# Optimization experiments

Measured on AMD Instinct MI355X. Metric: run time of the kernel, lower is better.

The kernel has to match this reference:

```python
import jax, jax.numpy as jnp
import numpy as np

N_NODES = 100000
FT_IN = 128
NHID = 64
N_EDGES = 1000000


def setup_inputs() -> dict:
    key = jax.random.key(0)
    ks = jax.random.split(key, 9)
    seq = jax.random.normal(ks[0], (N_NODES, FT_IN), dtype=jnp.float32)
    row = jax.random.randint(ks[1], (N_EDGES,), 0, N_NODES, dtype=jnp.int32)
    col = jax.random.randint(ks[2], (N_EDGES,), 0, N_NODES, dtype=jnp.int32)
    # encoder: LogReg Linear(ft_in, nhid), xavier-uniform weight, zero bias
    lim_enc = float(np.sqrt(6.0 / (FT_IN + NHID)))
    W_enc = jax.random.uniform(ks[3], (NHID, FT_IN), jnp.float32, -lim_enc, lim_enc)
    b_enc = jnp.zeros((NHID,), jnp.float32)
    # decoder lin1: Linear(2*nhid, nhid)
    lim1 = float(1.0 / np.sqrt(2 * NHID))
    W1 = jax.random.uniform(ks[4], (NHID, 2 * NHID), jnp.float32, -lim1, lim1)
    b1 = jax.random.uniform(ks[5], (NHID,), jnp.float32, -lim1, lim1)
    # decoder lin2: Linear(nhid, 1)
    lim2 = float(1.0 / np.sqrt(NHID))
    W2 = jax.random.uniform(ks[6], (1, NHID), jnp.float32, -lim2, lim2)
    b2 = jax.random.uniform(ks[7], (1,), jnp.float32, -lim2, lim2)
    return {"seq": seq, "W_enc": W_enc, "b_enc": b_enc, "W1": W1, "b1": b1,
            "W2": W2, "b2": b2, "row": row, "col": col}


def reference(seq, W_enc, b_enc, W1, b1, W2, b2, row, col):
    # encoder: z_all = seq @ W_enc^T + b_enc   -> [N, nhid]
    z = seq @ W_enc.T + b_enc
    # edge gather + concat -> [E, 2*nhid]
    e = jnp.concatenate([z[row], z[col]], axis=-1)
    h = jax.nn.relu(e @ W1.T + b1)             # [E, nhid]
    out = h @ W2.T + b2                        # [E, 1]
    return out.reshape(-1)
```

## Files before the change

### kernel.cpp

```cpp
#include <hip/hip_runtime.h>
#include <hip/hip_bf16.h>


#define K_IN  128
#define N_OUT 128
#define LDB   136

typedef short bf16x8 __attribute__((ext_vector_type(8)));
typedef float f32x4  __attribute__((ext_vector_type(4)));
typedef _Float16 half8 __attribute__((ext_vector_type(8)));

static __device__ __forceinline__ short f2bf(float x) {
    __hip_bfloat16 h = __float2bfloat16(x);
    return *reinterpret_cast<short*>(&h);
}

__global__ __launch_bounds__(256) void prep_kernel(
        const float* __restrict__ W_enc, const float* __restrict__ b_enc,
        const float* __restrict__ W1,    const float* __restrict__ b1,
        __hip_bfloat16* __restrict__ Wb, float* __restrict__ bcat)
{
    int idx = blockIdx.x * blockDim.x + threadIdx.x;
    if (idx >= N_OUT * K_IN) return;
    int i = idx >> 7;
    int k = idx & 127;
    int irow = i & 63;
    int joff = (i < 64) ? 0 : 64;
    float s = 0.f;
    #pragma unroll 8
    for (int j = 0; j < 64; ++j)
        s = fmaf(W1[irow * 128 + joff + j], W_enc[j * 128 + k], s);
    Wb[i * K_IN + k] = __float2bfloat16(s);
    if (k == 0) {
        float b = 0.f;
        for (int j = 0; j < 64; ++j)
            b = fmaf(W1[irow * 128 + joff + j], b_enc[j], b);
        if (i < 64) b += b1[i];
        bcat[i] = b;
    }
}

__global__ __launch_bounds__(256) void node_proj_kernel(
        const float* __restrict__ seq, const __hip_bfloat16* __restrict__ Wb,
        const float* __restrict__ bcat, _Float16* __restrict__ UVh, int nNodes)
{
    __shared__ short Bs[N_OUT * LDB];

    int tid  = threadIdx.x;
    int base = blockIdx.x * 64;

    #pragma unroll
    for (int it = 0; it < 8; ++it) {
        int c8 = tid + 256 * it;
        int r  = c8 >> 4;
        int cb = (c8 & 15) * 8;
        *(int4*)(Bs + r * LDB + cb) = *(const int4*)(Wb + r * K_IN + cb);
    }
    __syncthreads();

    int lane = tid & 63;
    int w    = tid >> 6;
    int lr   = lane & 15;
    int lg   = lane >> 4;

    int arow = base + 16 * w + lr;
    if (arow >= nNodes) arow = nNodes - 1;
    const float* aptr = seq + (size_t)arow * K_IN + lg * 8;

    f32x4 acc[8];
    #pragma unroll
    for (int nt = 0; nt < 8; ++nt) {
        float b = bcat[nt * 16 + lr];
        acc[nt] = (f32x4){b, b, b, b};
    }

    #pragma unroll
    for (int kk = 0; kk < 4; ++kk) {
        float4 f0 = *(const float4*)(aptr + kk * 32);
        float4 f1 = *(const float4*)(aptr + kk * 32 + 4);
        bf16x8 a;
        a[0] = f2bf(f0.x); a[1] = f2bf(f0.y); a[2] = f2bf(f0.z); a[3] = f2bf(f0.w);
        a[4] = f2bf(f1.x); a[5] = f2bf(f1.y); a[6] = f2bf(f1.z); a[7] = f2bf(f1.w);
        #pragma unroll
        for (int nt = 0; nt < 8; ++nt) {
            bf16x8 b = *(bf16x8*)(Bs + (nt * 16 + lr) * LDB + kk * 32 + lg * 8);
            acc[nt] = __builtin_amdgcn_mfma_f32_16x16x32_bf16(a, b, acc[nt], 0, 0, 0);
        }
    }

    int nodeb = base + 16 * w + lg * 4;
    #pragma unroll
    for (int j = 0; j < 4; ++j) {
        int node = nodeb + j;
        if (node < nNodes) {
            #pragma unroll
            for (int nt = 0; nt < 8; ++nt)
                UVh[(size_t)node * N_OUT + nt * 16 + lr] = (_Float16)acc[nt][j];
        }
    }
}

__global__ __launch_bounds__(256) void edge_kernel(
        const _Float16* __restrict__ UVh, const int* __restrict__ row,
        const int* __restrict__ col, const float* __restrict__ W2,
        const float* __restrict__ b2, float* __restrict__ out, int nEdges)
{
    int l = threadIdx.x & 7;
    float w2v[8];
    #pragma unroll
    for (int j = 0; j < 8; ++j) w2v[j] = W2[l * 8 + j];
    float bb = b2[0];

    int gid = (int)((blockIdx.x * blockDim.x + threadIdx.x) >> 3);
    int ng  = (int)((gridDim.x * blockDim.x) >> 3);

    for (int e0 = gid * 4; e0 < nEdges; e0 += ng * 4) {
        if (e0 + 4 <= nEdges) {
            int4 r4 = *(const int4*)(row + e0);
            int4 c4 = *(const int4*)(col + e0);
            half8 a0 = *(const half8*)(UVh + (size_t)r4.x * N_OUT + l * 8);
            half8 b0 = *(const half8*)(UVh + (size_t)c4.x * N_OUT + 64 + l * 8);
            half8 a1 = *(const half8*)(UVh + (size_t)r4.y * N_OUT + l * 8);
            half8 b1 = *(const half8*)(UVh + (size_t)c4.y * N_OUT + 64 + l * 8);
            half8 a2 = *(const half8*)(UVh + (size_t)r4.z * N_OUT + l * 8);
            half8 b2v = *(const half8*)(UVh + (size_t)c4.z * N_OUT + 64 + l * 8);
            half8 a3 = *(const half8*)(UVh + (size_t)r4.w * N_OUT + l * 8);
            half8 b3 = *(const half8*)(UVh + (size_t)c4.w * N_OUT + 64 + l * 8);

            float p0 = 0.f, p1 = 0.f, p2 = 0.f, p3 = 0.f;
            #pragma unroll
            for (int j = 0; j < 8; ++j) {
                p0 = fmaf(fmaxf((float)a0[j] + (float)b0[j], 0.f), w2v[j], p0);
                p1 = fmaf(fmaxf((float)a1[j] + (float)b1[j], 0.f), w2v[j], p1);
                p2 = fmaf(fmaxf((float)a2[j] + (float)b2v[j], 0.f), w2v[j], p2);
                p3 = fmaf(fmaxf((float)a3[j] + (float)b3[j], 0.f), w2v[j], p3);
            }
            #pragma unroll
            for (int s = 1; s < 8; s <<= 1) {
                p0 += __shfl_xor(p0, s);
                p1 += __shfl_xor(p1, s);
                p2 += __shfl_xor(p2, s);
                p3 += __shfl_xor(p3, s);
            }
            if (l == 0)
                *(float4*)(out + e0) = make_float4(p0 + bb, p1 + bb, p2 + bb, p3 + bb);
        } else {
            for (int e = e0; e < nEdges; ++e) {
                int r = row[e];
                int c = col[e];
                half8 a = *(const half8*)(UVh + (size_t)r * N_OUT + l * 8);
                half8 b = *(const half8*)(UVh + (size_t)c * N_OUT + 64 + l * 8);
                float p = 0.f;
                #pragma unroll
                for (int j = 0; j < 8; ++j)
                    p = fmaf(fmaxf((float)a[j] + (float)b[j], 0.f), w2v[j], p);
                #pragma unroll
                for (int s = 1; s < 8; s <<= 1) p += __shfl_xor(p, s);
                if (l == 0) out[e] = p + bb;
            }
        }
    }
}

extern "C" void kernel_launch(void* const* d_in, const int* in_sizes, int n_in,
                              void* d_out, int out_size, void* d_ws, size_t ws_size,
                              hipStream_t stream) {
    const float* seq   = (const float*)d_in[0];
    const float* W_enc = (const float*)d_in[1];
    const float* b_enc = (const float*)d_in[2];
    const float* W1    = (const float*)d_in[3];
    const float* b1    = (const float*)d_in[4];
    const float* W2    = (const float*)d_in[5];
    const float* b2    = (const float*)d_in[6];
    const int*   row   = (const int*)d_in[7];
    const int*   col   = (const int*)d_in[8];
    float* out = (float*)d_out;

    int nNodes = in_sizes[0] / K_IN;
    int nEdges = in_sizes[7];

    _Float16* UVh = (_Float16*)d_ws;
    __hip_bfloat16* Wb = (__hip_bfloat16*)((char*)d_ws +
                         (size_t)nNodes * N_OUT * sizeof(_Float16));
    float* bcat = (float*)((char*)Wb + N_OUT * K_IN * sizeof(__hip_bfloat16));

    prep_kernel<<<(N_OUT * K_IN + 255) / 256, 256, 0, stream>>>(
        W_enc, b_enc, W1, b1, Wb, bcat);

    int nblocksA = (nNodes + 63) / 64;
    node_proj_kernel<<<nblocksA, 256, 0, stream>>>(seq, Wb, bcat, UVh, nNodes);

    edge_kernel<<<2048, 256, 0, stream>>>(UVh, row, col, W2, b2, out, nEdges);
}
```

Before: 59.85 us.

## Persist node projection over tiles, vectorize permuted fp16 stores, nontemporal edge output

The node projection kernel now loops over two tiles per block, so the shared-memory weight load is amortized over more rows. Its output columns are permuted so each lane writes contiguous half4 vectors instead of scattered scalar halves. The edge kernel reads W2 through the matching permutation, uses 32-bit index arithmetic, and writes its output with nontemporal stores. In exchange the node kernel launches half as many blocks, which lowers parallelism, and it relies on the layout permutation staying consistent between the two kernels.

```diff
diff --git a/kernel.cpp b/kernel.cpp
--- a/kernel.cpp
+++ b/kernel.cpp
@@ -9,6 +9,8 @@
 typedef short bf16x8 __attribute__((ext_vector_type(8)));
 typedef float f32x4  __attribute__((ext_vector_type(4)));
 typedef _Float16 half8 __attribute__((ext_vector_type(8)));
+typedef _Float16 half4v __attribute__((ext_vector_type(4)));
+typedef float fv4   __attribute__((ext_vector_type(4)));
 
 static __device__ __forceinline__ short f2bf(float x) {
     __hip_bfloat16 h = __float2bfloat16(x);
@@ -42,12 +44,12 @@
 
 __global__ __launch_bounds__(256) void node_proj_kernel(
         const float* __restrict__ seq, const __hip_bfloat16* __restrict__ Wb,
-        const float* __restrict__ bcat, _Float16* __restrict__ UVh, int nNodes)
+        const float* __restrict__ bcat, _Float16* __restrict__ UVh,
+        int nNodes, int nTiles)
 {
     __shared__ short Bs[N_OUT * LDB];
 
-    int tid  = threadIdx.x;
-    int base = blockIdx.x * 64;
+    int tid = threadIdx.x;
 
     #pragma unroll
     for (int it = 0; it < 8; ++it) {
@@ -63,39 +65,47 @@
     int lr   = lane & 15;
     int lg   = lane >> 4;
 
-    int arow = base + 16 * w + lr;
-    if (arow >= nNodes) arow = nNodes - 1;
-    const float* aptr = seq + (size_t)arow * K_IN + lg * 8;
-
-    f32x4 acc[8];
+    float bias[8];
     #pragma unroll
-    for (int nt = 0; nt < 8; ++nt) {
-        float b = bcat[nt * 16 + lr];
-        acc[nt] = (f32x4){b, b, b, b};
-    }
-
-    #pragma unroll
-    for (int kk = 0; kk < 4; ++kk) {
-        float4 f0 = *(const float4*)(aptr + kk * 32);
-        float4 f1 = *(const float4*)(aptr + kk * 32 + 4);
-        bf16x8 a;
-        a[0] = f2bf(f0.x); a[1] = f2bf(f0.y); a[2] = f2bf(f0.z); a[3] = f2bf(f0.w);
-        a[4] = f2bf(f1.x); a[5] = f2bf(f1.y); a[6] = f2bf(f1.z); a[7] = f2bf(f1.w);
+    for (int nt = 0; nt < 8; ++nt) bias[nt] = bcat[nt * 16 + lr];
+
+    for (int tile = blockIdx.x; tile < nTiles; tile += gridDim.x) {
+        int base = tile * 64;
+        int arow = base + 16 * w + lr;
+        if (arow >= nNodes) arow = nNodes - 1;
+        const float* aptr = seq + (size_t)arow * K_IN + lg * 8;
+
+        f32x4 acc[8];
         #pragma unroll
-        for (int nt = 0; nt < 8; ++nt) {
-            bf16x8 b = *(bf16x8*)(Bs + (nt * 16 + lr) * LDB + kk * 32 + lg * 8);
-            acc[nt] = __builtin_amdgcn_mfma_f32_16x16x32_bf16(a, b, acc[nt], 0, 0, 0);
+        for (int nt = 0; nt < 8; ++nt)
+            acc[nt] = (f32x4){bias[nt], bias[nt], bias[nt], bias[nt]};
+
+        #pragma unroll
+        for (int kk = 0; kk < 4; ++kk) {
+            float4 f0 = *(const float4*)(aptr + kk * 32);
+            float4 f1 = *(const float4*)(aptr + kk * 32 + 4);
+            bf16x8 a;
+            a[0] = f2bf(f0.x); a[1] = f2bf(f0.y); a[2] = f2bf(f0.z); a[3] = f2bf(f0.w);
+            a[4] = f2bf(f1.x); a[5] = f2bf(f1.y); a[6] = f2bf(f1.z); a[7] = f2bf(f1.w);
+            #pragma unroll
+            for (int nt = 0; nt < 8; ++nt) {
+                bf16x8 b = *(bf16x8*)(Bs + (nt * 16 + lr) * LDB + kk * 32 + lg * 8);
+                acc[nt] = __builtin_amdgcn_mfma_f32_16x16x32_bf16(a, b, acc[nt], 0, 0, 0);
+            }
         }
-    }
-
-    int nodeb = base + 16 * w + lg * 4;
-    #pragma unroll
-    for (int j = 0; j < 4; ++j) {
-        int node = nodeb + j;
-        if (node < nNodes) {
-            #pragma unroll
-            for (int nt = 0; nt < 8; ++nt)
-                UVh[(size_t)node * N_OUT + nt * 16 + lr] = (_Float16)acc[nt][j];
+
+        int nodeb = base + 16 * w + lg * 4;
+        #pragma unroll
+        for (int j = 0; j < 4; ++j) {
+            int node = nodeb + j;
+            if (node < nNodes) {
+                half4v u = {(_Float16)acc[0][j], (_Float16)acc[1][j],
+                            (_Float16)acc[2][j], (_Float16)acc[3][j]};
+                half4v v = {(_Float16)acc[4][j], (_Float16)acc[5][j],
+                            (_Float16)acc[6][j], (_Float16)acc[7][j]};
+                *(half4v*)(UVh + (size_t)node * N_OUT + lr * 4)      = u;
+                *(half4v*)(UVh + (size_t)node * N_OUT + 64 + lr * 4) = v;
+            }
         }
     }
 }
@@ -108,7 +118,10 @@
     int l = threadIdx.x & 7;
     float w2v[8];
     #pragma unroll
-    for (int j = 0; j < 8; ++j) w2v[j] = W2[l * 8 + j];
+    for (int j = 0; j < 8; ++j) {
+        int p = l * 8 + j;
+        w2v[j] = W2[(p & 3) * 16 + (p >> 2)];
+    }
     float bb = b2[0];
 
     int gid = (int)((blockIdx.x * blockDim.x + threadIdx.x) >> 3);
@@ -118,14 +131,14 @@
         if (e0 + 4 <= nEdges) {
             int4 r4 = *(const int4*)(row + e0);
             int4 c4 = *(const int4*)(col + e0);
-            half8 a0 = *(const half8*)(UVh + (size_t)r4.x * N_OUT + l * 8);
-            half8 b0 = *(const half8*)(UVh + (size_t)c4.x * N_OUT + 64 + l * 8);
-            half8 a1 = *(const half8*)(UVh + (size_t)r4.y * N_OUT + l * 8);
-            half8 b1 = *(const half8*)(UVh + (size_t)c4.y * N_OUT + 64 + l * 8);
-            half8 a2 = *(const half8*)(UVh + (size_t)r4.z * N_OUT + l * 8);
-            half8 b2v = *(const half8*)(UVh + (size_t)c4.z * N_OUT + 64 + l * 8);
-            half8 a3 = *(const half8*)(UVh + (size_t)r4.w * N_OUT + l * 8);
-            half8 b3 = *(const half8*)(UVh + (size_t)c4.w * N_OUT + 64 + l * 8);
+            half8 a0 = *(const half8*)(UVh + ((unsigned)r4.x << 7) + l * 8);
+            half8 b0 = *(const half8*)(UVh + ((unsigned)c4.x << 7) + 64 + l * 8);
+            half8 a1 = *(const half8*)(UVh + ((unsigned)r4.y << 7) + l * 8);
+            half8 b1 = *(const half8*)(UVh + ((unsigned)c4.y << 7) + 64 + l * 8);
+            half8 a2 = *(const half8*)(UVh + ((unsigned)r4.z << 7) + l * 8);
+            half8 b2v = *(const half8*)(UVh + ((unsigned)c4.z << 7) + 64 + l * 8);
+            half8 a3 = *(const half8*)(UVh + ((unsigned)r4.w << 7) + l * 8);
+            half8 b3 = *(const half8*)(UVh + ((unsigned)c4.w << 7) + 64 + l * 8);
 
             float p0 = 0.f, p1 = 0.f, p2 = 0.f, p3 = 0.f;
             #pragma unroll
@@ -142,14 +155,16 @@
                 p2 += __shfl_xor(p2, s);
                 p3 += __shfl_xor(p3, s);
             }
-            if (l == 0)
-                *(float4*)(out + e0) = make_float4(p0 + bb, p1 + bb, p2 + bb, p3 + bb);
+            if (l == 0) {
+                fv4 o = {p0 + bb, p1 + bb, p2 + bb, p3 + bb};
+                __builtin_nontemporal_store(o, (fv4*)(out + e0));
+            }
         } else {
             for (int e = e0; e < nEdges; ++e) {
                 int r = row[e];
                 int c = col[e];
-                half8 a = *(const half8*)(UVh + (size_t)r * N_OUT + l * 8);
-                half8 b = *(const half8*)(UVh + (size_t)c * N_OUT + 64 + l * 8);
+                half8 a = *(const half8*)(UVh + ((unsigned)r << 7) + l * 8);
+                half8 b = *(const half8*)(UVh + ((unsigned)c << 7) + 64 + l * 8);
                 float p = 0.f;
                 #pragma unroll
                 for (int j = 0; j < 8; ++j)
@@ -187,8 +202,9 @@
     prep_kernel<<<(N_OUT * K_IN + 255) / 256, 256, 0, stream>>>(
         W_enc, b_enc, W1, b1, Wb, bcat);
 
-    int nblocksA = (nNodes + 63) / 64;
-    node_proj_kernel<<<nblocksA, 256, 0, stream>>>(seq, Wb, bcat, UVh, nNodes);
+    int nTiles = (nNodes + 63) / 64;
+    int nblocksA = (nTiles + 1) / 2;
+    node_proj_kernel<<<nblocksA, 256, 0, stream>>>(seq, Wb, bcat, UVh, nNodes, nTiles);
 
     edge_kernel<<<2048, 256, 0, stream>>>(UVh, row, col, W2, b2, out, nEdges);
 }
```

Measured after the change: 60.05 us. Within noise of the previous version (+0.3%).
